# Performance work log

Hardware: AMD Instinct MI355X
Metric: run time of the kernel (lower is better)

Reference implementation:

```python
import math
import jax, jax.numpy as jnp
import numpy as np

NODE_DIM = 256
EDGE_DIM = 64
NUM_HEADS = 8
ATTN_DIM = NODE_DIM // NUM_HEADS


def setup_inputs() -> dict:
    key = jax.random.key(0)
    ks = jax.random.split(key, 12)
    B, N = 2, 256
    s_node = 1.0 / math.sqrt(NODE_DIM)
    s_edge = 1.0 / math.sqrt(EDGE_DIM)
    return {
        "nodes": jax.random.normal(ks[0], (B, N, NODE_DIM), jnp.float32),
        "edges": jax.random.normal(ks[1], (B, N, N, EDGE_DIM), jnp.float32),
        "W_qkv": jax.random.normal(ks[2], (NODE_DIM, 3 * NODE_DIM), jnp.float32) * s_node,
        "b_qkv": jax.random.normal(ks[3], (3 * NODE_DIM,), jnp.float32) * 0.01,
        "W_ss": jax.random.normal(ks[4], (EDGE_DIM, 2 * NODE_DIM), jnp.float32) * s_edge,
        "b_ss": jax.random.normal(ks[5], (2 * NODE_DIM,), jnp.float32) * 0.01,
        "W_nodes": jax.random.normal(ks[6], (NODE_DIM, NODE_DIM), jnp.float32) * s_node,
        "b_nodes": jax.random.normal(ks[7], (NODE_DIM,), jnp.float32) * 0.01,
        "W_edges": jax.random.normal(ks[8], (NODE_DIM, EDGE_DIM), jnp.float32) * s_node,
        "b_edges": jax.random.normal(ks[9], (EDGE_DIM,), jnp.float32) * 0.01,
    }


def reference(nodes, edges, W_qkv, b_qkv, W_ss, b_ss, W_nodes, b_nodes, W_edges, b_edges):
    B, N, _ = nodes.shape
    H, D = NUM_HEADS, ATTN_DIM

    qkv = nodes @ W_qkv + b_qkv                      # [B,N,3*node_dim]
    q, k, v = jnp.split(qkv, 3, axis=-1)
    q = q.reshape(B, N, H, D).transpose(0, 2, 1, 3)  # [B,H,N,D]
    k = k.reshape(B, N, H, D).transpose(0, 2, 1, 3)
    v = v.reshape(B, N, H, D).transpose(0, 2, 1, 3)

    # explicit outer product: [B,H,Nq,Nk,D]
    attn = q[:, :, :, None, :] * k[:, :, None, :, :]

    ss = edges @ W_ss + b_ss                         # [B,N,N,2*node_dim]
    shift, scale = jnp.split(ss, 2, axis=-1)
    shift = shift.reshape(B, N, N, H, D).transpose(0, 3, 1, 2, 4)  # [B,H,N,N,D]
    scale = scale.reshape(B, N, N, H, D).transpose(0, 3, 1, 2, 4)

    new_edges = attn * scale + attn + shift          # [B,H,Nq,Nk,D]

    logits = new_edges.sum(axis=4) / math.sqrt(D)    # [B,H,Nq,Nk]
    # NOTE: original softmaxes over dim=2 (the query axis) — reproduced faithfully
    attention = jax.nn.softmax(logits, axis=2)

    # intended math of `attention @ values` then head-merge
    weighted = jnp.einsum('bhqk,bhkd->bqhd', attention, v).reshape(B, N, H * D)

    edge_feat = new_edges.transpose(0, 2, 3, 1, 4).reshape(B, N, N, H * D)

    new_nodes = weighted @ W_nodes + b_nodes
    new_edges_out = jax.nn.leaky_relu(edge_feat, negative_slope=0.1) @ W_edges + b_edges
    return new_nodes, new_edges_out
```

## Files before the change

kernel.cpp:

```cpp
#include <hip/hip_runtime.h>


typedef unsigned short ushortT;
typedef short s16x8 __attribute__((ext_vector_type(8)));
typedef float f32x4 __attribute__((ext_vector_type(4)));

#define MFMA16(a, b, c) __builtin_amdgcn_mfma_f32_16x16x32_bf16(a, b, c, 0, 0, 0)

#define CF4(p) (*reinterpret_cast<const float4*>(p))
#define F4(p)  (*reinterpret_cast<float4*>(p))

__device__ __forceinline__ ushortT f2bf(float x) {
  union { float f; unsigned u; } v; v.f = x;
  unsigned r = (v.u + 0x7FFFu + ((v.u >> 16) & 1u)) >> 16;
  return (ushortT)r;
}
__device__ __forceinline__ float bf2f(ushortT h) {
  union { unsigned u; float f; } v; v.u = ((unsigned)h) << 16;
  return v.f;
}

__global__ __launch_bounds__(256) void prep_weights(
    const float* __restrict__ W_ss, const float* __restrict__ W_edges,
    ushortT* __restrict__ WssT_h, ushortT* __restrict__ WssT_l,
    ushortT* __restrict__ WeT_h,  ushortT* __restrict__ WeT_l)
{
  const int idx = blockIdx.x * 256 + threadIdx.x;
  for (int e = idx; e < 512 * 64; e += 16384) {
    const int c = e >> 6, i = e & 63;
    const float x = W_ss[i * 512 + c];
    const ushortT h = f2bf(x);
    WssT_h[e] = h;
    WssT_l[e] = f2bf(x - bf2f(h));
  }
  for (int e = idx; e < 64 * 256; e += 16384) {
    const int j = e >> 8, c = e & 255;
    const float x = W_edges[c * 64 + j];
    const ushortT h = f2bf(x);
    WeT_h[e] = h;
    WeT_l[e] = f2bf(x - bf2f(h));
  }
}

__global__ __launch_bounds__(256) void gemm_bias_kernel(
    const float* __restrict__ A, const float* __restrict__ B,
    const float* __restrict__ bias, float* __restrict__ C,
    int M, int Nn, int K)
{
  __shared__ float As[16][68];
  __shared__ float Bs[16][68];
  const int t  = threadIdx.x;
  const int nbx = Nn >> 6;
  const int bx = blockIdx.x % nbx;
  const int by = blockIdx.x / nbx;
  const int r0 = by << 6, c0 = bx << 6;
  const int tx = t & 15, ty = t >> 4;
  float acc[4][4];
#pragma unroll
  for (int i = 0; i < 4; ++i)
#pragma unroll
    for (int j = 0; j < 4; ++j) acc[i][j] = 0.f;

  for (int kt = 0; kt < K; kt += 16) {
    {
      const int r = t >> 2, k4 = (t & 3) << 2;
      const float4 a = CF4(A + (size_t)(r0 + r) * K + kt + k4);
      As[k4 + 0][r] = a.x; As[k4 + 1][r] = a.y; As[k4 + 2][r] = a.z; As[k4 + 3][r] = a.w;
    }
    {
      const int kk = t >> 4, c4 = (t & 15) << 2;
      F4(&Bs[kk][c4]) = CF4(B + (size_t)(kt + kk) * Nn + c0 + c4);
    }
    __syncthreads();
#pragma unroll
    for (int kk = 0; kk < 16; ++kk) {
      const float4 av = F4(&As[kk][ty << 2]);
      const float4 bv = F4(&Bs[kk][tx << 2]);
      const float aa[4] = {av.x, av.y, av.z, av.w};
      const float bb[4] = {bv.x, bv.y, bv.z, bv.w};
#pragma unroll
      for (int rr = 0; rr < 4; ++rr)
#pragma unroll
        for (int cc = 0; cc < 4; ++cc)
          acc[rr][cc] = fmaf(aa[rr], bb[cc], acc[rr][cc]);
    }
    __syncthreads();
  }
  const float4 bv = CF4(bias + c0 + (tx << 2));
  const float bb[4] = {bv.x, bv.y, bv.z, bv.w};
#pragma unroll
  for (int rr = 0; rr < 4; ++rr) {
    float4 o;
    o.x = acc[rr][0] + bb[0]; o.y = acc[rr][1] + bb[1];
    o.z = acc[rr][2] + bb[2]; o.w = acc[rr][3] + bb[3];
    F4(C + (size_t)(r0 + (ty << 2) + rr) * Nn + c0 + (tx << 2)) = o;
  }
}

__global__ __launch_bounds__(256, 2) void edge_mfma_kernel(
    const float* __restrict__ edges, const float* __restrict__ qkv,
    const ushortT* __restrict__ WssT_h, const ushortT* __restrict__ WssT_l,
    const float* __restrict__ b_ss,
    const ushortT* __restrict__ WeT_h, const ushortT* __restrict__ WeT_l,
    const float* __restrict__ b_edges,
    float* __restrict__ out_edges, float* __restrict__ logits)
{
  __shared__ ushortT Eh[128 * 64];
  __shared__ ushortT El[128 * 64];
  __shared__ ushortT Nh[128 * 64];
  __shared__ ushortT Nl[128 * 64];
  __shared__ float qv_l[256];

  const int t    = threadIdx.x;
  const int lane = t & 63;
  const int w    = t >> 6;
  const int l15  = lane & 15;
  const int lg   = lane >> 4;
  const int bid  = blockIdx.x;
  const int kh   = bid & 1;
  const int q    = (bid >> 1) & 255;
  const int b    = bid >> 9;
  const int k0   = kh << 7;
  const int rw   = w << 5;

  qv_l[t] = qkv[(size_t)(b * 256 + q) * 768 + t];

  const float* eBase = edges + ((size_t)((b * 256 + q) * 256 + k0)) * 64;
#pragma unroll
  for (int u = 0; u < 8; ++u) {
    const int f = t + u * 256;
    const int r = f >> 4, i4 = (f & 15) << 2;
    const float4 v = CF4(eBase + r * 64 + i4);
    const ushortT h0 = f2bf(v.x), h1 = f2bf(v.y), h2 = f2bf(v.z), h3 = f2bf(v.w);
    const ushortT e0 = f2bf(v.x - bf2f(h0)), e1 = f2bf(v.y - bf2f(h1)),
                  e2 = f2bf(v.z - bf2f(h2)), e3 = f2bf(v.w - bf2f(h3));
    int byte = r * 128 + i4 * 2; byte ^= (r & 7) << 4;
    *reinterpret_cast<ushort4*>(reinterpret_cast<char*>(Eh) + byte) = make_ushort4(h0, h1, h2, h3);
    *reinterpret_cast<ushort4*>(reinterpret_cast<char*>(El) + byte) = make_ushort4(e0, e1, e2, e3);
  }
  __syncthreads();

  const f32x4 zero4 = {0.f, 0.f, 0.f, 0.f};
  f32x4 accO[2][4];
#pragma unroll
  for (int rt = 0; rt < 2; ++rt)
#pragma unroll
    for (int jt = 0; jt < 4; ++jt) accO[rt][jt] = zero4;

  for (int ch = 0; ch < 4; ++ch) {
    const int c0 = ch << 6;

    f32x4 accS[2][4], accC[2][4];
#pragma unroll
    for (int ct = 0; ct < 4; ++ct) {
      const float bs = b_ss[c0 + ct * 16 + l15];
      const float bc = b_ss[256 + c0 + ct * 16 + l15];
      f32x4 vs = {bs, bs, bs, bs}, vc = {bc, bc, bc, bc};
      accS[0][ct] = vs; accS[1][ct] = vs;
      accC[0][ct] = vc; accC[1][ct] = vc;
    }

#pragma unroll
    for (int ks = 0; ks < 2; ++ks) {
      s16x8 bsh[4], bsl[4], bch[4], bcl[4];
#pragma unroll
      for (int ct = 0; ct < 4; ++ct) {
        const size_t off = (size_t)(c0 + ct * 16 + l15) * 64 + 32 * ks + 8 * lg;
        bsh[ct] = *reinterpret_cast<const s16x8*>(WssT_h + off);
        bsl[ct] = *reinterpret_cast<const s16x8*>(WssT_l + off);
        bch[ct] = *reinterpret_cast<const s16x8*>(WssT_h + off + 256 * 64);
        bcl[ct] = *reinterpret_cast<const s16x8*>(WssT_l + off + 256 * 64);
      }
#pragma unroll
      for (int rt = 0; rt < 2; ++rt) {
        const int row = rw + rt * 16 + l15;
        int byte = row * 128 + (32 * ks + 8 * lg) * 2; byte ^= (row & 7) << 4;
        const s16x8 ah = *reinterpret_cast<const s16x8*>(reinterpret_cast<const char*>(Eh) + byte);
        const s16x8 al = *reinterpret_cast<const s16x8*>(reinterpret_cast<const char*>(El) + byte);
#pragma unroll
        for (int ct = 0; ct < 4; ++ct) {
          accS[rt][ct] = MFMA16(ah, bsh[ct], accS[rt][ct]);
          accS[rt][ct] = MFMA16(ah, bsl[ct], accS[rt][ct]);
          accS[rt][ct] = MFMA16(al, bsh[ct], accS[rt][ct]);
          accC[rt][ct] = MFMA16(ah, bch[ct], accC[rt][ct]);
          accC[rt][ct] = MFMA16(ah, bcl[ct], accC[rt][ct]);
          accC[rt][ct] = MFMA16(al, bch[ct], accC[rt][ct]);
        }
      }
    }

    float lgacc[2][2][4];
#pragma unroll
    for (int rt = 0; rt < 2; ++rt)
#pragma unroll
      for (int hh = 0; hh < 2; ++hh)
#pragma unroll
        for (int r = 0; r < 4; ++r) lgacc[rt][hh][r] = 0.f;

#pragma unroll
    for (int rt = 0; rt < 2; ++rt) {
#pragma unroll
      for (int ct = 0; ct < 4; ++ct) {
        const float qvc = qv_l[c0 + ct * 16 + l15];
        const float* kvp = qkv + (size_t)(b * 256 + k0 + rw + rt * 16 + lg * 4) * 768
                               + 256 + c0 + ct * 16 + l15;
#pragma unroll
        for (int r = 0; r < 4; ++r) {
          const float kvv = kvp[(size_t)r * 768];
          const float a  = qvc * kvv;
          const float ne = fmaf(a, accC[rt][ct][r], a) + accS[rt][ct][r];
          lgacc[rt][ct >> 1][r] += ne;
          const float nel = ne > 0.f ? ne : 0.1f * ne;
          const ushortT nh = f2bf(nel);
          const ushortT nl = f2bf(nel - bf2f(nh));
          const int row = rw + rt * 16 + lg * 4 + r;
          int byte = row * 128 + (ct * 16 + l15) * 2; byte ^= (row & 7) << 4;
          *reinterpret_cast<ushortT*>(reinterpret_cast<char*>(Nh) + byte) = nh;
          *reinterpret_cast<ushortT*>(reinterpret_cast<char*>(Nl) + byte) = nl;
        }
      }
    }

#pragma unroll
    for (int rt = 0; rt < 2; ++rt)
#pragma unroll
      for (int hh = 0; hh < 2; ++hh)
#pragma unroll
        for (int r = 0; r < 4; ++r) {
          float v = lgacc[rt][hh][r];
          v += __shfl_xor(v, 1);
          v += __shfl_xor(v, 2);
          v += __shfl_xor(v, 4);
          v += __shfl_xor(v, 8);
          lgacc[rt][hh][r] = v;
        }
    if (l15 == 0) {
#pragma unroll
      for (int rt = 0; rt < 2; ++rt)
#pragma unroll
        for (int hh = 0; hh < 2; ++hh) {
          float4 o;
          o.x = lgacc[rt][hh][0] * 0.17677669529663687f;
          o.y = lgacc[rt][hh][1] * 0.17677669529663687f;
          o.z = lgacc[rt][hh][2] * 0.17677669529663687f;
          o.w = lgacc[rt][hh][3] * 0.17677669529663687f;
          const int h = ch * 2 + hh;
          const int krow = k0 + rw + rt * 16 + lg * 4;
          F4(logits + ((size_t)((b * 8 + h) * 256 + q)) * 256 + krow) = o;
        }
    }

#pragma unroll
    for (int ks = 0; ks < 2; ++ks) {
      s16x8 wh[4], wl[4];
#pragma unroll
      for (int jt = 0; jt < 4; ++jt) {
        const size_t off = (size_t)(jt * 16 + l15) * 256 + c0 + 32 * ks + 8 * lg;
        wh[jt] = *reinterpret_cast<const s16x8*>(WeT_h + off);
        wl[jt] = *reinterpret_cast<const s16x8*>(WeT_l + off);
      }
#pragma unroll
      for (int rt = 0; rt < 2; ++rt) {
        const int row = rw + rt * 16 + l15;
        int byte = row * 128 + (32 * ks + 8 * lg) * 2; byte ^= (row & 7) << 4;
        const s16x8 anh = *reinterpret_cast<const s16x8*>(reinterpret_cast<const char*>(Nh) + byte);
        const s16x8 anl = *reinterpret_cast<const s16x8*>(reinterpret_cast<const char*>(Nl) + byte);
#pragma unroll
        for (int jt = 0; jt < 4; ++jt) {
          accO[rt][jt] = MFMA16(anh, wh[jt], accO[rt][jt]);
          accO[rt][jt] = MFMA16(anh, wl[jt], accO[rt][jt]);
          accO[rt][jt] = MFMA16(anl, wh[jt], accO[rt][jt]);
        }
      }
    }
  }

#pragma unroll
  for (int rt = 0; rt < 2; ++rt)
#pragma unroll
    for (int jt = 0; jt < 4; ++jt) {
      const float be = b_edges[jt * 16 + l15];
#pragma unroll
      for (int r = 0; r < 4; ++r) {
        const int krow = k0 + rw + rt * 16 + lg * 4 + r;
        out_edges[((size_t)((b * 256 + q) * 256 + krow)) * 64 + jt * 16 + l15] =
            accO[rt][jt][r] + be;
      }
    }
}

__global__ __launch_bounds__(256) void softmax_stats_kernel(
    const float* __restrict__ logits, float* __restrict__ mOut, float* __restrict__ rOut)
{
  __shared__ float sm[8][33], sx[8][33];
  const int bh = blockIdx.x >> 3, kc = blockIdx.x & 7;
  const int kl = threadIdx.x & 31, qg = threadIdx.x >> 5;
  const float* base = logits + (size_t)bh * 65536 + kc * 32 + kl;
  float arr[32];
#pragma unroll
  for (int i = 0; i < 32; ++i) arr[i] = base[(size_t)(qg * 32 + i) * 256];
  float m = arr[0];
#pragma unroll
  for (int i = 1; i < 32; ++i) m = fmaxf(m, arr[i]);
  float s = 0.f;
#pragma unroll
  for (int i = 0; i < 32; ++i) s += __expf(arr[i] - m);
  sm[qg][kl] = m; sx[qg][kl] = s;
  __syncthreads();
  if (threadIdx.x < 32) {
    float M = sm[0][kl];
#pragma unroll
    for (int g = 1; g < 8; ++g) M = fmaxf(M, sm[g][kl]);
    float S = 0.f;
#pragma unroll
    for (int g = 0; g < 8; ++g) S += sx[g][kl] * __expf(sm[g][kl] - M);
    mOut[bh * 256 + kc * 32 + kl] = M;
    rOut[bh * 256 + kc * 32 + kl] = 1.f / S;
  }
}

__global__ __launch_bounds__(256) void weighted_fused_kernel(
    const float* __restrict__ logits, const float* __restrict__ mOut,
    const float* __restrict__ rOut, const float* __restrict__ qkv,
    float* __restrict__ weighted)
{
  __shared__ float P[32][260];
  __shared__ float mc[256], rc[256];
  const int qt = blockIdx.x & 7, h = (blockIdx.x >> 3) & 7, b = blockIdx.x >> 6;
  const int bh = b * 8 + h;
  const int t = threadIdx.x;
  mc[t] = mOut[bh * 256 + t];
  rc[t] = rOut[bh * 256 + t];
  __syncthreads();
  const float* lb = logits + (size_t)bh * 65536 + (size_t)qt * 32 * 256;
#pragma unroll
  for (int u = 0; u < 8; ++u) {
    const int f = t + u * 256;
    const int qq = f >> 6, k4 = (f & 63) << 2;
    const float4 v = CF4(lb + qq * 256 + k4);
    P[qq][k4 + 0] = __expf(v.x - mc[k4 + 0]) * rc[k4 + 0];
    P[qq][k4 + 1] = __expf(v.y - mc[k4 + 1]) * rc[k4 + 1];
    P[qq][k4 + 2] = __expf(v.z - mc[k4 + 2]) * rc[k4 + 2];
    P[qq][k4 + 3] = __expf(v.w - mc[k4 + 3]) * rc[k4 + 3];
  }
  __syncthreads();
  const int dg = t & 7, qq = t >> 3;
  const float* vb = qkv + (size_t)b * 196608 + 512 + h * 32 + dg * 4;
  float a0 = 0.f, a1 = 0.f, a2 = 0.f, a3 = 0.f;
#pragma unroll 4
  for (int k = 0; k < 256; ++k) {
    const float p = P[qq][k];
    const float4 v = CF4(vb + (size_t)k * 768);
    a0 = fmaf(p, v.x, a0); a1 = fmaf(p, v.y, a1);
    a2 = fmaf(p, v.z, a2); a3 = fmaf(p, v.w, a3);
  }
  float4 o; o.x = a0; o.y = a1; o.z = a2; o.w = a3;
  F4(weighted + ((size_t)(b * 256 + qt * 32 + qq)) * 256 + h * 32 + dg * 4) = o;
}

extern "C" void kernel_launch(void* const* d_in, const int* in_sizes, int n_in,
                              void* d_out, int out_size, void* d_ws, size_t ws_size,
                              hipStream_t stream) {
  const float* nodes   = (const float*)d_in[0];
  const float* edges   = (const float*)d_in[1];
  const float* W_qkv   = (const float*)d_in[2];
  const float* b_qkv   = (const float*)d_in[3];
  const float* W_ss    = (const float*)d_in[4];
  const float* b_ss    = (const float*)d_in[5];
  const float* W_nodes = (const float*)d_in[6];
  const float* b_nodes = (const float*)d_in[7];
  const float* W_edges = (const float*)d_in[8];
  const float* b_edges = (const float*)d_in[9];

  float* out_nodes = (float*)d_out;
  float* out_edges = out_nodes + 131072;

  float* wsf      = (float*)d_ws;
  float* qkv      = wsf;
  float* logits   = wsf + 393216;
  float* weighted = wsf + 1441792;
  float* mcol     = wsf + 1572864;
  float* rcol     = wsf + 1576960;
  ushortT* wss    = (ushortT*)(wsf + 1581056);
  ushortT* WssT_h = wss;
  ushortT* WssT_l = wss + 32768;
  ushortT* WeT_h  = wss + 65536;
  ushortT* WeT_l  = wss + 81920;

  prep_weights<<<64, 256, 0, stream>>>(W_ss, W_edges, WssT_h, WssT_l, WeT_h, WeT_l);
  gemm_bias_kernel<<<96, 256, 0, stream>>>(nodes, W_qkv, b_qkv, qkv, 512, 768, 256);
  edge_mfma_kernel<<<1024, 256, 0, stream>>>(edges, qkv, WssT_h, WssT_l, b_ss,
                                             WeT_h, WeT_l, b_edges, out_edges, logits);
  softmax_stats_kernel<<<128, 256, 0, stream>>>(logits, mcol, rcol);
  weighted_fused_kernel<<<128, 256, 0, stream>>>(logits, mcol, rcol, qkv, weighted);
  gemm_bias_kernel<<<32, 256, 0, stream>>>(weighted, W_nodes, b_nodes, out_nodes, 512, 256, 256);
}
```

Before: 263.5 us.

## Use 512-thread edge blocks, fuse qkv GEMM with weight prep, smaller GEMM tiles

```diff
diff --git a/kernel.cpp b/kernel.cpp
--- a/kernel.cpp
+++ b/kernel.cpp
@@ -8,6 +8,7 @@
 #define MFMA16(a, b, c) __builtin_amdgcn_mfma_f32_16x16x32_bf16(a, b, c, 0, 0, 0)
 
 #define CF4(p) (*reinterpret_cast<const float4*>(p))
+#define CF2(p) (*reinterpret_cast<const float2*>(p))
 #define F4(p)  (*reinterpret_cast<float4*>(p))
 
 __device__ __forceinline__ ushortT f2bf(float x) {
@@ -20,12 +21,73 @@
   return v.f;
 }
 
-__global__ __launch_bounds__(256) void prep_weights(
+__device__ __forceinline__ void gemm32_body(
+    const float* __restrict__ A, const float* __restrict__ B,
+    const float* __restrict__ bias, float* __restrict__ C,
+    int Nn, int K, int blk)
+{
+  __shared__ float As[16][36];
+  __shared__ float Bs[16][68];
+  const int t  = threadIdx.x;
+  const int nbx = Nn >> 6;
+  const int bx = blk % nbx;
+  const int by = blk / nbx;
+  const int r0 = by << 5, c0 = bx << 6;
+  const int tx = t & 15, ty = t >> 4;
+  float acc[2][4];
+#pragma unroll
+  for (int i = 0; i < 2; ++i)
+#pragma unroll
+    for (int j = 0; j < 4; ++j) acc[i][j] = 0.f;
+
+  for (int kt = 0; kt < K; kt += 16) {
+    {
+      const int r = t >> 3, k2 = (t & 7) << 1;
+      const float2 a = CF2(A + (size_t)(r0 + r) * K + kt + k2);
+      As[k2 + 0][r] = a.x; As[k2 + 1][r] = a.y;
+    }
+    {
+      const int kk = t >> 4, c4 = (t & 15) << 2;
+      F4(&Bs[kk][c4]) = CF4(B + (size_t)(kt + kk) * Nn + c0 + c4);
+    }
+    __syncthreads();
+#pragma unroll
+    for (int kk = 0; kk < 16; ++kk) {
+      const float a0 = As[kk][ty * 2 + 0];
+      const float a1 = As[kk][ty * 2 + 1];
+      const float4 bv = F4(&Bs[kk][tx << 2]);
+      const float bb[4] = {bv.x, bv.y, bv.z, bv.w};
+#pragma unroll
+      for (int cc = 0; cc < 4; ++cc) {
+        acc[0][cc] = fmaf(a0, bb[cc], acc[0][cc]);
+        acc[1][cc] = fmaf(a1, bb[cc], acc[1][cc]);
+      }
+    }
+    __syncthreads();
+  }
+  const float4 bv = CF4(bias + c0 + (tx << 2));
+  const float bb[4] = {bv.x, bv.y, bv.z, bv.w};
+#pragma unroll
+  for (int rr = 0; rr < 2; ++rr) {
+    float4 o;
+    o.x = acc[rr][0] + bb[0]; o.y = acc[rr][1] + bb[1];
+    o.z = acc[rr][2] + bb[2]; o.w = acc[rr][3] + bb[3];
+    F4(C + (size_t)(r0 + ty * 2 + rr) * Nn + c0 + (tx << 2)) = o;
+  }
+}
+
+__global__ __launch_bounds__(256) void qkv_prep_kernel(
+    const float* __restrict__ nodes, const float* __restrict__ W_qkv,
+    const float* __restrict__ b_qkv, float* __restrict__ qkv,
     const float* __restrict__ W_ss, const float* __restrict__ W_edges,
     ushortT* __restrict__ WssT_h, ushortT* __restrict__ WssT_l,
     ushortT* __restrict__ WeT_h,  ushortT* __restrict__ WeT_l)
 {
-  const int idx = blockIdx.x * 256 + threadIdx.x;
+  if (blockIdx.x < 192) {
+    gemm32_body(nodes, W_qkv, b_qkv, qkv, 768, 256, blockIdx.x);
+    return;
+  }
+  const int idx = (blockIdx.x - 192) * 256 + threadIdx.x;
   for (int e = idx; e < 512 * 64; e += 16384) {
     const int c = e >> 6, i = e & 63;
     const float x = W_ss[i * 512 + c];
@@ -42,62 +104,14 @@
   }
 }
 
-__global__ __launch_bounds__(256) void gemm_bias_kernel(
+__global__ __launch_bounds__(256) void gemm32_kernel(
     const float* __restrict__ A, const float* __restrict__ B,
-    const float* __restrict__ bias, float* __restrict__ C,
-    int M, int Nn, int K)
-{
-  __shared__ float As[16][68];
-  __shared__ float Bs[16][68];
-  const int t  = threadIdx.x;
-  const int nbx = Nn >> 6;
-  const int bx = blockIdx.x % nbx;
-  const int by = blockIdx.x / nbx;
-  const int r0 = by << 6, c0 = bx << 6;
-  const int tx = t & 15, ty = t >> 4;
-  float acc[4][4];
-#pragma unroll
-  for (int i = 0; i < 4; ++i)
-#pragma unroll
-    for (int j = 0; j < 4; ++j) acc[i][j] = 0.f;
-
-  for (int kt = 0; kt < K; kt += 16) {
-    {
-      const int r = t >> 2, k4 = (t & 3) << 2;
-      const float4 a = CF4(A + (size_t)(r0 + r) * K + kt + k4);
-      As[k4 + 0][r] = a.x; As[k4 + 1][r] = a.y; As[k4 + 2][r] = a.z; As[k4 + 3][r] = a.w;
-    }
-    {
-      const int kk = t >> 4, c4 = (t & 15) << 2;
-      F4(&Bs[kk][c4]) = CF4(B + (size_t)(kt + kk) * Nn + c0 + c4);
-    }
-    __syncthreads();
-#pragma unroll
-    for (int kk = 0; kk < 16; ++kk) {
-      const float4 av = F4(&As[kk][ty << 2]);
-      const float4 bv = F4(&Bs[kk][tx << 2]);
-      const float aa[4] = {av.x, av.y, av.z, av.w};
-      const float bb[4] = {bv.x, bv.y, bv.z, bv.w};
-#pragma unroll
-      for (int rr = 0; rr < 4; ++rr)
-#pragma unroll
-        for (int cc = 0; cc < 4; ++cc)
-          acc[rr][cc] = fmaf(aa[rr], bb[cc], acc[rr][cc]);
-    }
-    __syncthreads();
-  }
-  const float4 bv = CF4(bias + c0 + (tx << 2));
-  const float bb[4] = {bv.x, bv.y, bv.z, bv.w};
-#pragma unroll
-  for (int rr = 0; rr < 4; ++rr) {
-    float4 o;
-    o.x = acc[rr][0] + bb[0]; o.y = acc[rr][1] + bb[1];
-    o.z = acc[rr][2] + bb[2]; o.w = acc[rr][3] + bb[3];
-    F4(C + (size_t)(r0 + (ty << 2) + rr) * Nn + c0 + (tx << 2)) = o;
-  }
-}
-
-__global__ __launch_bounds__(256, 2) void edge_mfma_kernel(
+    const float* __restrict__ bias, float* __restrict__ C, int Nn, int K)
+{
+  gemm32_body(A, B, bias, C, Nn, K, blockIdx.x);
+}
+
+__global__ __launch_bounds__(512, 4) void edge_mfma_kernel(
     const float* __restrict__ edges, const float* __restrict__ qkv,
     const ushortT* __restrict__ WssT_h, const ushortT* __restrict__ WssT_l,
     const float* __restrict__ b_ss,
@@ -121,14 +135,14 @@
   const int q    = (bid >> 1) & 255;
   const int b    = bid >> 9;
   const int k0   = kh << 7;
-  const int rw   = w << 5;
-
-  qv_l[t] = qkv[(size_t)(b * 256 + q) * 768 + t];
+  const int rw   = w << 4;
+
+  if (t < 256) qv_l[t] = qkv[(size_t)(b * 256 + q) * 768 + t];
 
   const float* eBase = edges + ((size_t)((b * 256 + q) * 256 + k0)) * 64;
 #pragma unroll
-  for (int u = 0; u < 8; ++u) {
-    const int f = t + u * 256;
+  for (int u = 0; u < 4; ++u) {
+    const int f = t + u * 512;
     const int r = f >> 4, i4 = (f & 15) << 2;
     const float4 v = CF4(eBase + r * 64 + i4);
     const ushortT h0 = f2bf(v.x), h1 = f2bf(v.y), h2 = f2bf(v.z), h3 = f2bf(v.w);
@@ -141,152 +155,124 @@
   __syncthreads();
 
   const f32x4 zero4 = {0.f, 0.f, 0.f, 0.f};
-  f32x4 accO[2][4];
-#pragma unroll
-  for (int rt = 0; rt < 2; ++rt)
-#pragma unroll
-    for (int jt = 0; jt < 4; ++jt) accO[rt][jt] = zero4;
+  f32x4 accO[4];
+#pragma unroll
+  for (int jt = 0; jt < 4; ++jt) accO[jt] = zero4;
 
   for (int ch = 0; ch < 4; ++ch) {
     const int c0 = ch << 6;
 
-    f32x4 accS[2][4], accC[2][4];
+    f32x4 accS[4], accC[4];
 #pragma unroll
     for (int ct = 0; ct < 4; ++ct) {
       const float bs = b_ss[c0 + ct * 16 + l15];
       const float bc = b_ss[256 + c0 + ct * 16 + l15];
-      f32x4 vs = {bs, bs, bs, bs}, vc = {bc, bc, bc, bc};
-      accS[0][ct] = vs; accS[1][ct] = vs;
-      accC[0][ct] = vc; accC[1][ct] = vc;
+      const f32x4 vs = {bs, bs, bs, bs}, vc = {bc, bc, bc, bc};
+      accS[ct] = vs; accC[ct] = vc;
     }
 
 #pragma unroll
     for (int ks = 0; ks < 2; ++ks) {
-      s16x8 bsh[4], bsl[4], bch[4], bcl[4];
+      const int row = rw + l15;
+      int abyte = row * 128 + (32 * ks + 8 * lg) * 2; abyte ^= (row & 7) << 4;
+      const s16x8 ah = *reinterpret_cast<const s16x8*>(reinterpret_cast<const char*>(Eh) + abyte);
+      const s16x8 al = *reinterpret_cast<const s16x8*>(reinterpret_cast<const char*>(El) + abyte);
 #pragma unroll
       for (int ct = 0; ct < 4; ++ct) {
         const size_t off = (size_t)(c0 + ct * 16 + l15) * 64 + 32 * ks + 8 * lg;
-        bsh[ct] = *reinterpret_cast<const s16x8*>(WssT_h + off);
-        bsl[ct] = *reinterpret_cast<const s16x8*>(WssT_l + off);
-        bch[ct] = *reinterpret_cast<const s16x8*>(WssT_h + off + 256 * 64);
-        bcl[ct] = *reinterpret_cast<const s16x8*>(WssT_l + off + 256 * 64);
-      }
-#pragma unroll
-      for (int rt = 0; rt < 2; ++rt) {
-        const int row = rw + rt * 16 + l15;
-        int byte = row * 128 + (32 * ks + 8 * lg) * 2; byte ^= (row & 7) << 4;
-        const s16x8 ah = *reinterpret_cast<const s16x8*>(reinterpret_cast<const char*>(Eh) + byte);
-        const s16x8 al = *reinterpret_cast<const s16x8*>(reinterpret_cast<const char*>(El) + byte);
-#pragma unroll
-        for (int ct = 0; ct < 4; ++ct) {
-          accS[rt][ct] = MFMA16(ah, bsh[ct], accS[rt][ct]);
-          accS[rt][ct] = MFMA16(ah, bsl[ct], accS[rt][ct]);
-          accS[rt][ct] = MFMA16(al, bsh[ct], accS[rt][ct]);
-          accC[rt][ct] = MFMA16(ah, bch[ct], accC[rt][ct]);
-          accC[rt][ct] = MFMA16(ah, bcl[ct], accC[rt][ct]);
-          accC[rt][ct] = MFMA16(al, bch[ct], accC[rt][ct]);
-        }
-      }
-    }
-
-    float lgacc[2][2][4];
-#pragma unroll
-    for (int rt = 0; rt < 2; ++rt)
-#pragma unroll
-      for (int hh = 0; hh < 2; ++hh)
-#pragma unroll
-        for (int r = 0; r < 4; ++r) lgacc[rt][hh][r] = 0.f;
-
-#pragma unroll
-    for (int rt = 0; rt < 2; ++rt) {
-#pragma unroll
-      for (int ct = 0; ct < 4; ++ct) {
-        const float qvc = qv_l[c0 + ct * 16 + l15];
-        const float* kvp = qkv + (size_t)(b * 256 + k0 + rw + rt * 16 + lg * 4) * 768
-                               + 256 + c0 + ct * 16 + l15;
-#pragma unroll
-        for (int r = 0; r < 4; ++r) {
-          const float kvv = kvp[(size_t)r * 768];
-          const float a  = qvc * kvv;
-          const float ne = fmaf(a, accC[rt][ct][r], a) + accS[rt][ct][r];
-          lgacc[rt][ct >> 1][r] += ne;
-          const float nel = ne > 0.f ? ne : 0.1f * ne;
-          const ushortT nh = f2bf(nel);
-          const ushortT nl = f2bf(nel - bf2f(nh));
-          const int row = rw + rt * 16 + lg * 4 + r;
-          int byte = row * 128 + (ct * 16 + l15) * 2; byte ^= (row & 7) << 4;
-          *reinterpret_cast<ushortT*>(reinterpret_cast<char*>(Nh) + byte) = nh;
-          *reinterpret_cast<ushortT*>(reinterpret_cast<char*>(Nl) + byte) = nl;
-        }
-      }
-    }
-
-#pragma unroll
-    for (int rt = 0; rt < 2; ++rt)
-#pragma unroll
-      for (int hh = 0; hh < 2; ++hh)
-#pragma unroll
-        for (int r = 0; r < 4; ++r) {
-          float v = lgacc[rt][hh][r];
-          v += __shfl_xor(v, 1);
-          v += __shfl_xor(v, 2);
-          v += __shfl_xor(v, 4);
-          v += __shfl_xor(v, 8);
-          lgacc[rt][hh][r] = v;
-        }
+        const s16x8 bsh = *reinterpret_cast<const s16x8*>(WssT_h + off);
+        const s16x8 bsl = *reinterpret_cast<const s16x8*>(WssT_l + off);
+        const s16x8 bch = *reinterpret_cast<const s16x8*>(WssT_h + off + 16384);
+        const s16x8 bcl = *reinterpret_cast<const s16x8*>(WssT_l + off + 16384);
+        accS[ct] = MFMA16(ah, bsh, accS[ct]);
+        accS[ct] = MFMA16(ah, bsl, accS[ct]);
+        accS[ct] = MFMA16(al, bsh, accS[ct]);
+        accC[ct] = MFMA16(ah, bch, accC[ct]);
+        accC[ct] = MFMA16(ah, bcl, accC[ct]);
+        accC[ct] = MFMA16(al, bch, accC[ct]);
+      }
+    }
+
+    float lgacc[2][4];
+#pragma unroll
+    for (int hh = 0; hh < 2; ++hh)
+#pragma unroll
+      for (int r = 0; r < 4; ++r) lgacc[hh][r] = 0.f;
+
+#pragma unroll
+    for (int ct = 0; ct < 4; ++ct) {
+      const float qvc = qv_l[c0 + ct * 16 + l15];
+      const float* kvp = qkv + (size_t)(b * 256 + k0 + rw + lg * 4) * 768
+                             + 256 + c0 + ct * 16 + l15;
+#pragma unroll
+      for (int r = 0; r < 4; ++r) {
+        const float kvv = kvp[(size_t)r * 768];
+        const float a  = qvc * kvv;
+        const float ne = fmaf(a, accC[ct][r], a) + accS[ct][r];
+        lgacc[ct >> 1][r] += ne;
+        const float nel = ne > 0.f ? ne : 0.1f * ne;
+        const ushortT nh = f2bf(nel);
+        const ushortT nl = f2bf(nel - bf2f(nh));
+        const int row = rw + lg * 4 + r;
+        int byte = row * 128 + (ct * 16 + l15) * 2; byte ^= (row & 7) << 4;
+        *reinterpret_cast<ushortT*>(reinterpret_cast<char*>(Nh) + byte) = nh;
+        *reinterpret_cast<ushortT*>(reinterpret_cast<char*>(Nl) + byte) = nl;
+      }
+    }
+
+#pragma unroll
+    for (int hh = 0; hh < 2; ++hh)
+#pragma unroll
+      for (int r = 0; r < 4; ++r) {
+        float v = lgacc[hh][r];
+        v += __shfl_xor(v, 1);
+        v += __shfl_xor(v, 2);
+        v += __shfl_xor(v, 4);
+        v += __shfl_xor(v, 8);
+        lgacc[hh][r] = v;
+      }
     if (l15 == 0) {
 #pragma unroll
-      for (int rt = 0; rt < 2; ++rt)
-#pragma unroll
-        for (int hh = 0; hh < 2; ++hh) {
-          float4 o;
-          o.x = lgacc[rt][hh][0] * 0.17677669529663687f;
-          o.y = lgacc[rt][hh][1] * 0.17677669529663687f;
-          o.z = lgacc[rt][hh][2] * 0.17677669529663687f;
-          o.w = lgacc[rt][hh][3] * 0.17677669529663687f;
-          const int h = ch * 2 + hh;
-          const int krow = k0 + rw + rt * 16 + lg * 4;
-          F4(logits + ((size_t)((b * 8 + h) * 256 + q)) * 256 + krow) = o;
-        }
+      for (int hh = 0; hh < 2; ++hh) {
+        float4 o;
+        o.x = lgacc[hh][0] * 0.17677669529663687f;
+        o.y = lgacc[hh][1] * 0.17677669529663687f;
+        o.z = lgacc[hh][2] * 0.17677669529663687f;
+        o.w = lgacc[hh][3] * 0.17677669529663687f;
+        const int h = ch * 2 + hh;
+        const int krow = k0 + rw + lg * 4;
+        F4(logits + ((size_t)((b * 8 + h) * 256 + q)) * 256 + krow) = o;
+      }
     }
 
 #pragma unroll
     for (int ks = 0; ks < 2; ++ks) {
-      s16x8 wh[4], wl[4];
+      const int row = rw + l15;
+      int abyte = row * 128 + (32 * ks + 8 * lg) * 2; abyte ^= (row & 7) << 4;
+      const s16x8 anh = *reinterpret_cast<const s16x8*>(reinterpret_cast<const char*>(Nh) + abyte);
+      const s16x8 anl = *reinterpret_cast<const s16x8*>(reinterpret_cast<const char*>(Nl) + abyte);
 #pragma unroll
       for (int jt = 0; jt < 4; ++jt) {
         const size_t off = (size_t)(jt * 16 + l15) * 256 + c0 + 32 * ks + 8 * lg;
-        wh[jt] = *reinterpret_cast<const s16x8*>(WeT_h + off);
-        wl[jt] = *reinterpret_cast<const s16x8*>(WeT_l + off);
-      }
-#pragma unroll
-      for (int rt = 0; rt < 2; ++rt) {
-        const int row = rw + rt * 16 + l15;
-        int byte = row * 128 + (32 * ks + 8 * lg) * 2; byte ^= (row & 7) << 4;
-        const s16x8 anh = *reinterpret_cast<const s16x8*>(reinterpret_cast<const char*>(Nh) + byte);
-        const s16x8 anl = *reinterpret_cast<const s16x8*>(reinterpret_cast<const char*>(Nl) + byte);
-#pragma unroll
-        for (int jt = 0; jt < 4; ++jt) {
-          accO[rt][jt] = MFMA16(anh, wh[jt], accO[rt][jt]);
-          accO[rt][jt] = MFMA16(anh, wl[jt], accO[rt][jt]);
-          accO[rt][jt] = MFMA16(anl, wh[jt], accO[rt][jt]);
-        }
-      }
-    }
-  }
-
-#pragma unroll
-  for (int rt = 0; rt < 2; ++rt)
-#pragma unroll
-    for (int jt = 0; jt < 4; ++jt) {
-      const float be = b_edges[jt * 16 + l15];
-#pragma unroll
-      for (int r = 0; r < 4; ++r) {
-        const int krow = k0 + rw + rt * 16 + lg * 4 + r;
-        out_edges[((size_t)((b * 256 + q) * 256 + krow)) * 64 + jt * 16 + l15] =
-            accO[rt][jt][r] + be;
-      }
-    }
+        const s16x8 wh = *reinterpret_cast<const s16x8*>(WeT_h + off);
+        const s16x8 wl = *reinterpret_cast<const s16x8*>(WeT_l + off);
+        accO[jt] = MFMA16(anh, wh, accO[jt]);
+        accO[jt] = MFMA16(anh, wl, accO[jt]);
+        accO[jt] = MFMA16(anl, wh, accO[jt]);
+      }
+    }
+  }
+
+#pragma unroll
+  for (int jt = 0; jt < 4; ++jt) {
+    const float be = b_edges[jt * 16 + l15];
+#pragma unroll
+    for (int r = 0; r < 4; ++r) {
+      const int krow = k0 + rw + lg * 4 + r;
+      out_edges[((size_t)((b * 256 + q) * 256 + krow)) * 64 + jt * 16 + l15] =
+          accO[jt][r] + be;
+    }
+  }
 }
 
 __global__ __launch_bounds__(256) void softmax_stats_kernel(
@@ -387,11 +373,11 @@
   ushortT* WeT_h  = wss + 65536;
   ushortT* WeT_l  = wss + 81920;
 
-  prep_weights<<<64, 256, 0, stream>>>(W_ss, W_edges, WssT_h, WssT_l, WeT_h, WeT_l);
-  gemm_bias_kernel<<<96, 256, 0, stream>>>(nodes, W_qkv, b_qkv, qkv, 512, 768, 256);
-  edge_mfma_kernel<<<1024, 256, 0, stream>>>(edges, qkv, WssT_h, WssT_l, b_ss,
+  qkv_prep_kernel<<<256, 256, 0, stream>>>(nodes, W_qkv, b_qkv, qkv,
+                                           W_ss, W_edges, WssT_h, WssT_l, WeT_h, WeT_l);
+  edge_mfma_kernel<<<1024, 512, 0, stream>>>(edges, qkv, WssT_h, WssT_l, b_ss,
                                              WeT_h, WeT_l, b_edges, out_edges, logits);
   softmax_stats_kernel<<<128, 256, 0, stream>>>(logits, mcol, rcol);
   weighted_fused_kernel<<<128, 256, 0, stream>>>(logits, mcol, rcol, qkv, weighted);
-  gemm_bias_kernel<<<32, 256, 0, stream>>>(weighted, W_nodes, b_nodes, out_nodes, 512, 256, 256);
-}
+  gemm32_kernel<<<64, 256, 0, stream>>>(weighted, W_nodes, b_nodes, out_nodes, 256, 256);
+}
```

New measurement: 362.4 us. +37.6%, slower.
